# Performance work log

Hardware: AMD Instinct MI355X
Metric: run time of the kernel (lower is better)

Reference implementation:

```python
import jax, jax.numpy as jnp
import numpy as np

B, C, D, H, W = 2, 128, 16, 16, 16

def setup_inputs() -> dict:
    key = jax.random.key(0)
    ks = jax.random.split(key, 7)
    s = 0.02
    return {
        "x": jax.random.normal(ks[0], (B, C, D, H, W), jnp.float32),
        "Wq": jax.random.normal(ks[1], (C, C), jnp.float32) * s,
        "bq": jax.random.normal(ks[2], (C,), jnp.float32) * s,
        "Wk": jax.random.normal(ks[3], (C, C), jnp.float32) * s,
        "bk": jax.random.normal(ks[4], (C,), jnp.float32) * s,
        "Wv": jax.random.normal(ks[5], (C, C), jnp.float32) * s,
        "bv": jax.random.normal(ks[6], (C,), jnp.float32) * s,
    }

def reference(x, Wq, bq, Wk, bk, Wv, bv):
    b, c, d, h, w = x.shape
    n = d * h * w
    xf = x.reshape(b, c, n)  # [B, C, N]
    # 1x1x1 Conv3d == per-voxel linear over channels
    q = jnp.einsum('oc,bcn->bon', Wq, xf) + bq[None, :, None]
    k = jnp.einsum('oc,bcn->bon', Wk, xf) + bk[None, :, None]
    v = jnp.einsum('oc,bcn->bon', Wv, xf) + bv[None, :, None]
    # energy[b,n,m] = sum_c q[b,c,n] * k[b,c,m]  (no scale, as in source)
    energy = jnp.einsum('bcn,bcm->bnm', q, k)
    attention = jax.nn.softmax(energy, axis=-1)
    # out[b,c,n] = sum_m v[b,c,m] * attention[b,n,m]
    out = jnp.einsum('bcm,bnm->bcn', v, attention)
    return out.reshape(b, c, d, h, w)
```

## Files before the change

kernel.cpp:

```cpp
#include <hip/hip_runtime.h>


typedef __bf16 bf16x8 __attribute__((ext_vector_type(8)));
typedef __bf16 bf16x4v __attribute__((ext_vector_type(4)));
typedef float  f32x4  __attribute__((ext_vector_type(4)));

#define LDP 136
#define LDV 72
#define LDO 33

constexpr int CB = 128;
constexpr int NB = 4096;
constexpr int BB = 2;

__device__ __forceinline__ bf16x8 ldfrag(const __bf16* lds, int row, int koff, int ld) {
  return *(const bf16x8*)(lds + row * ld + koff);
}

__device__ __forceinline__ unsigned cvt_pk_bf16(float lo, float hi) {
  unsigned w;
  asm("v_cvt_pk_bf16_f32 %0, %1, %2" : "=v"(w) : "v"(lo), "v"(hi));
  return w;
}

__global__ __launch_bounds__(256) void qkv_proj_kernel(
    const float* __restrict__ x,
    const float* __restrict__ Wq, const float* __restrict__ bq,
    const float* __restrict__ Wk, const float* __restrict__ bk,
    const float* __restrict__ Wv, const float* __restrict__ bv,
    __bf16* __restrict__ Qt, __bf16* __restrict__ Kt, __bf16* __restrict__ Vo)
{
  extern __shared__ __align__(16) char smem_raw[];
  __bf16* xT = (__bf16*)smem_raw;
  __bf16* Wl = xT + 64 * LDP;

  const int b  = blockIdx.y;
  const int n0 = blockIdx.x * 64;
  const int m  = blockIdx.z;
  const int t  = threadIdx.x;
  const int lane = t & 63, w = t >> 6;
  const int l15 = lane & 15, quad = lane >> 4;

  const float* W = (m == 0) ? Wq : (m == 1) ? Wk : Wv;
  const float* bias_p = (m == 0) ? bq : (m == 1) ? bk : bv;
  const float qscale = (m == 0) ? 1.4426950408889634f : 1.0f;

  for (int v = t; v < 2048; v += 256) {
    int c = v >> 4, i4 = v & 15;
    float4 d = *(const float4*)(x + (b * CB + c) * NB + n0 + i4 * 4);
    xT[(i4 * 4 + 0) * LDP + c] = (__bf16)d.x;
    xT[(i4 * 4 + 1) * LDP + c] = (__bf16)d.y;
    xT[(i4 * 4 + 2) * LDP + c] = (__bf16)d.z;
    xT[(i4 * 4 + 3) * LDP + c] = (__bf16)d.w;
  }
  for (int v = t; v < 4096; v += 256) {
    int o = v >> 5, c4 = v & 31;
    float4 d = *(const float4*)(W + o * 128 + c4 * 4);
    bf16x4v u = {(__bf16)d.x, (__bf16)d.y, (__bf16)d.z, (__bf16)d.w};
    *(bf16x4v*)(Wl + o * LDP + c4 * 4) = u;
  }
  __syncthreads();

  if (m < 2) {
    f32x4 acc[8];
#pragma unroll
    for (int ct = 0; ct < 8; ct++) acc[ct] = (f32x4)0.0f;
#pragma unroll
    for (int ks = 0; ks < 4; ks++) {
      int koff = ks * 32 + quad * 8;
      bf16x8 a = ldfrag(xT, w * 16 + l15, koff, LDP);
#pragma unroll
      for (int ct = 0; ct < 8; ct++) {
        bf16x8 bb = ldfrag(Wl, ct * 16 + l15, koff, LDP);
        acc[ct] = __builtin_amdgcn_mfma_f32_16x16x32_bf16(a, bb, acc[ct], 0, 0, 0);
      }
    }
    __bf16* O = (m == 0) ? Qt : Kt;
#pragma unroll
    for (int ct = 0; ct < 8; ct++) {
      int o = ct * 16 + l15;
      float bias = bias_p[o];
#pragma unroll
      for (int r = 0; r < 4; r++) {
        int i = w * 16 + quad * 4 + r;
        O[(b * NB + n0 + i) * CB + o] = (__bf16)((acc[ct][r] + bias) * qscale);
      }
    }
  } else {
    f32x4 acc[2][4];
#pragma unroll
    for (int rr = 0; rr < 2; rr++)
#pragma unroll
      for (int ct = 0; ct < 4; ct++) acc[rr][ct] = (f32x4)0.0f;
#pragma unroll
    for (int ks = 0; ks < 4; ks++) {
      int koff = ks * 32 + quad * 8;
      bf16x8 a0 = ldfrag(Wl, (w * 2 + 0) * 16 + l15, koff, LDP);
      bf16x8 a1 = ldfrag(Wl, (w * 2 + 1) * 16 + l15, koff, LDP);
#pragma unroll
      for (int ct = 0; ct < 4; ct++) {
        bf16x8 bb = ldfrag(xT, ct * 16 + l15, koff, LDP);
        acc[0][ct] = __builtin_amdgcn_mfma_f32_16x16x32_bf16(a0, bb, acc[0][ct], 0, 0, 0);
        acc[1][ct] = __builtin_amdgcn_mfma_f32_16x16x32_bf16(a1, bb, acc[1][ct], 0, 0, 0);
      }
    }
#pragma unroll
    for (int rr = 0; rr < 2; rr++)
#pragma unroll
      for (int ct = 0; ct < 4; ct++)
#pragma unroll
        for (int r = 0; r < 4; r++) {
          int o = (w * 2 + rr) * 16 + quad * 4 + r;
          int i = ct * 16 + l15;
          Vo[(b * CB + o) * NB + n0 + i] = (__bf16)(acc[rr][ct][r] + bias_p[o]);
        }
  }
}

__global__ __launch_bounds__(256, 2) void attn_part_kernel(
    const __bf16* __restrict__ Qt,
    const __bf16* __restrict__ Kt,
    const __bf16* __restrict__ Vo,
    __bf16* __restrict__ Opart, float* __restrict__ Ll, int ksz)
{
  extern __shared__ __align__(16) char smem_raw[];
  __bf16* Kl = (__bf16*)smem_raw;
  __bf16* Vl = Kl + 64 * LDP;
  __bf16* Pl = Vl + 128 * LDV;

  const int b  = blockIdx.y;
  const int q0 = blockIdx.x * 128;
  const int s  = blockIdx.z;
  const int k_base = s * ksz;
  const int nit = ksz >> 6;
  const int t  = threadIdx.x;
  const int lane = t & 63, w = t >> 6;
  const int l15 = lane & 15, quad = lane >> 4;
  const int row0 = w * 32;

  bf16x8 qf[2][4];
#pragma unroll
  for (int qt = 0; qt < 2; qt++)
#pragma unroll
    for (int cb = 0; cb < 4; cb++)
      qf[qt][cb] = *(const bf16x8*)(Qt +
          (size_t)(b * NB + q0 + row0 + qt * 16 + l15) * CB + cb * 32 + quad * 8);

#pragma unroll
  for (int u = 0; u < 4; u++) {
    int v = t + u * 256;
    int j = v >> 4, c8 = v & 15;
    *(bf16x8*)(Kl + j * LDP + c8 * 8) =
        *(const bf16x8*)(Kt + (size_t)(b * NB + k_base + j) * CB + c8 * 8);
  }
#pragma unroll
  for (int u = 0; u < 4; u++) {
    int v = t + u * 256;
    int c = v >> 3, j8 = v & 7;
    *(bf16x8*)(Vl + c * LDV + j8 * 8) =
        *(const bf16x8*)(Vo + (size_t)(b * CB + c) * NB + k_base + j8 * 8);
  }

  float lsum[2] = {0.0f, 0.0f};
  f32x4 o_acc[2][8];
#pragma unroll
  for (int qt = 0; qt < 2; qt++)
#pragma unroll
    for (int tt = 0; tt < 8; tt++) o_acc[qt][tt] = (f32x4)0.0f;

  __syncthreads();

  for (int it = 0; it < nit; it++) {
    bf16x8 kr[4], vr[4];
    if (it + 1 < nit) {
      int m1 = k_base + (it + 1) * 64;
#pragma unroll
      for (int u = 0; u < 4; u++) {
        int v = t + u * 256;
        int j = v >> 4, c8 = v & 15;
        kr[u] = *(const bf16x8*)(Kt + (size_t)(b * NB + m1 + j) * CB + c8 * 8);
      }
#pragma unroll
      for (int u = 0; u < 4; u++) {
        int v = t + u * 256;
        int c = v >> 3, j8 = v & 7;
        vr[u] = *(const bf16x8*)(Vo + (size_t)(b * CB + c) * NB + m1 + j8 * 8);
      }
    }

    f32x4 sacc[2][4];
#pragma unroll
    for (int qt = 0; qt < 2; qt++)
#pragma unroll
      for (int kt = 0; kt < 4; kt++) sacc[qt][kt] = (f32x4)0.0f;

    __builtin_amdgcn_s_setprio(1);
#pragma unroll
    for (int cb = 0; cb < 4; cb++) {
      int koff = cb * 32 + quad * 8;
#pragma unroll
      for (int kt = 0; kt < 4; kt++) {
        bf16x8 af = ldfrag(Kl, kt * 16 + l15, koff, LDP);
        sacc[0][kt] = __builtin_amdgcn_mfma_f32_16x16x32_bf16(af, qf[0][cb], sacc[0][kt], 0, 0, 0);
        sacc[1][kt] = __builtin_amdgcn_mfma_f32_16x16x32_bf16(af, qf[1][cb], sacc[1][kt], 0, 0, 0);
      }
    }
    __builtin_amdgcn_s_setprio(0);

#pragma unroll
    for (int qt = 0; qt < 2; qt++)
#pragma unroll
      for (int kt = 0; kt < 4; kt++) {
        float p0 = exp2f(sacc[qt][kt][0]);
        float p1 = exp2f(sacc[qt][kt][1]);
        float p2 = exp2f(sacc[qt][kt][2]);
        float p3 = exp2f(sacc[qt][kt][3]);
        lsum[qt] += (p0 + p1) + (p2 + p3);
        uint2 u;
        u.x = cvt_pk_bf16(p0, p1);
        u.y = cvt_pk_bf16(p2, p3);
        *(uint2*)(Pl + (row0 + qt * 16 + l15) * LDV + kt * 16 + quad * 4) = u;
      }
    asm volatile("s_waitcnt lgkmcnt(0)" ::: "memory");
    __builtin_amdgcn_sched_barrier(0);

    __builtin_amdgcn_s_setprio(1);
#pragma unroll
    for (int ks = 0; ks < 2; ks++) {
      int koff = ks * 32 + quad * 8;
      bf16x8 a0 = ldfrag(Pl, row0 + l15, koff, LDV);
      bf16x8 a1 = ldfrag(Pl, row0 + 16 + l15, koff, LDV);
#pragma unroll
      for (int tt = 0; tt < 8; tt++) {
        bf16x8 bb = ldfrag(Vl, tt * 16 + l15, koff, LDV);
        o_acc[0][tt] = __builtin_amdgcn_mfma_f32_16x16x32_bf16(a0, bb, o_acc[0][tt], 0, 0, 0);
        o_acc[1][tt] = __builtin_amdgcn_mfma_f32_16x16x32_bf16(a1, bb, o_acc[1][tt], 0, 0, 0);
      }
    }
    __builtin_amdgcn_s_setprio(0);

    if (it + 1 < nit) {
      __syncthreads();
#pragma unroll
      for (int u = 0; u < 4; u++) {
        int v = t + u * 256;
        int j = v >> 4, c8 = v & 15;
        *(bf16x8*)(Kl + j * LDP + c8 * 8) = kr[u];
      }
#pragma unroll
      for (int u = 0; u < 4; u++) {
        int v = t + u * 256;
        int c = v >> 3, j8 = v & 7;
        *(bf16x8*)(Vl + c * LDV + j8 * 8) = vr[u];
      }
      __syncthreads();
    }
  }

#pragma unroll
  for (int qt = 0; qt < 2; qt++) {
    lsum[qt] += __shfl_xor(lsum[qt], 16);
    lsum[qt] += __shfl_xor(lsum[qt], 32);
  }

  const size_t obase = ((size_t)(s * BB + b) * NB + q0) * CB;
#pragma unroll
  for (int qt = 0; qt < 2; qt++)
#pragma unroll
    for (int tt = 0; tt < 8; tt++)
#pragma unroll
      for (int r = 0; r < 4; r++)
        Opart[obase + (size_t)(row0 + qt * 16 + quad * 4 + r) * CB + tt * 16 + l15] =
            (__bf16)o_acc[qt][tt][r];
  if (quad == 0) {
    const size_t lbase = (size_t)(s * BB + b) * NB + q0 + row0;
#pragma unroll
    for (int qt = 0; qt < 2; qt++)
      Ll[lbase + qt * 16 + l15] = lsum[qt];
  }
}

__global__ __launch_bounds__(256) void combine_kernel(
    const __bf16* __restrict__ Opart, const float* __restrict__ Ll,
    float* __restrict__ out, int nsplit)
{
  extern __shared__ __align__(16) char smem_raw[];
  float* Olf = (float*)smem_raw;

  const int b  = blockIdx.y;
  const int n0 = blockIdx.x * 64;
  const int c0 = blockIdx.z * 32;
  const int t  = threadIdx.x;
  const int i  = t >> 2;
  const int cc = (t & 3) * 8;

  float L = 0.0f;
  for (int s = 0; s < nsplit; s++)
    L += Ll[(size_t)(s * BB + b) * NB + n0 + i];

  float acc[8];
#pragma unroll
  for (int u = 0; u < 8; u++) acc[u] = 0.0f;
  for (int s = 0; s < nsplit; s++) {
    bf16x8 d = *(const bf16x8*)(Opart +
        ((size_t)(s * BB + b) * NB + n0 + i) * CB + c0 + cc);
#pragma unroll
    for (int u = 0; u < 8; u++) acc[u] += (float)d[u];
  }
  float invL = 1.0f / L;
#pragma unroll
  for (int u = 0; u < 8; u++) Olf[i * LDO + cc + u] = acc[u] * invL;
  __syncthreads();

  for (int v = t; v < 512; v += 256) {
    int c = v >> 4, i4 = v & 15;
    float4 d;
    d.x = Olf[(i4 * 4 + 0) * LDO + c];
    d.y = Olf[(i4 * 4 + 1) * LDO + c];
    d.z = Olf[(i4 * 4 + 2) * LDO + c];
    d.w = Olf[(i4 * 4 + 3) * LDO + c];
    *(float4*)(out + (size_t)(b * CB + c0 + c) * NB + n0 + i4 * 4) = d;
  }
}

extern "C" void kernel_launch(void* const* d_in, const int* in_sizes, int n_in,
                              void* d_out, int out_size, void* d_ws, size_t ws_size,
                              hipStream_t stream) {
  const float* x  = (const float*)d_in[0];
  const float* Wq = (const float*)d_in[1];
  const float* bq = (const float*)d_in[2];
  const float* Wk = (const float*)d_in[3];
  const float* bk = (const float*)d_in[4];
  const float* Wv = (const float*)d_in[5];
  const float* bv = (const float*)d_in[6];
  float* out = (float*)d_out;

  const size_t qkv_elems = (size_t)BB * NB * CB;
  __bf16* Qt = (__bf16*)d_ws;
  __bf16* Kt = Qt + qkv_elems;
  __bf16* Vo = Kt + qkv_elems;
  char* ws_tail = (char*)(Vo + qkv_elems);
  size_t tail_sz = ws_size - 3 * qkv_elems * sizeof(__bf16);

  const size_t per_split = (size_t)BB * NB * CB * 2 + (size_t)BB * NB * 4;
  int nsplit = 8;
  while (nsplit > 1 && (size_t)nsplit * per_split > tail_sz) nsplit >>= 1;

  __bf16* Opart = (__bf16*)ws_tail;
  float*  Ll = (float*)(Opart + (size_t)nsplit * BB * NB * CB);
  const int ksz = NB / nsplit;

  const int qkv_smem  = (64 * LDP + 128 * LDP) * 2;
  const int attn_smem = (64 * LDP + 128 * LDV + 128 * LDV) * 2;
  const int comb_smem = 64 * LDO * 4;

  qkv_proj_kernel<<<dim3(NB / 64, BB, 3), 256, qkv_smem, stream>>>(
      x, Wq, bq, Wk, bk, Wv, bv, Qt, Kt, Vo);
  attn_part_kernel<<<dim3(NB / 128, BB, nsplit), 256, attn_smem, stream>>>(
      Qt, Kt, Vo, Opart, Ll, ksz);
  combine_kernel<<<dim3(NB / 64, BB, 4), 256, comb_smem, stream>>>(
      Opart, Ll, out, nsplit);
}
```

Measured before the change: 113.7 us.

## Double-buffer K/V tiles with XOR swizzle and keep P in registers via permlane

```diff
diff --git a/kernel.cpp b/kernel.cpp
--- a/kernel.cpp
+++ b/kernel.cpp
@@ -6,7 +6,6 @@
 typedef float  f32x4  __attribute__((ext_vector_type(4)));
 
 #define LDP 136
-#define LDV 72
 #define LDO 33
 
 constexpr int CB = 128;
@@ -124,9 +123,6 @@
     __bf16* __restrict__ Opart, float* __restrict__ Ll, int ksz)
 {
   extern __shared__ __align__(16) char smem_raw[];
-  __bf16* Kl = (__bf16*)smem_raw;
-  __bf16* Vl = Kl + 64 * LDP;
-  __bf16* Pl = Vl + 128 * LDV;
 
   const int b  = blockIdx.y;
   const int q0 = blockIdx.x * 128;
@@ -137,6 +133,7 @@
   const int lane = t & 63, w = t >> 6;
   const int l15 = lane & 15, quad = lane >> 4;
   const int row0 = w * 32;
+  const int xsw = (l15 & 7) << 4;
 
   bf16x8 qf[2][4];
 #pragma unroll
@@ -146,20 +143,37 @@
       qf[qt][cb] = *(const bf16x8*)(Qt +
           (size_t)(b * NB + q0 + row0 + qt * 16 + l15) * CB + cb * 32 + quad * 8);
 
-#pragma unroll
-  for (int u = 0; u < 4; u++) {
-    int v = t + u * 256;
-    int j = v >> 4, c8 = v & 15;
-    *(bf16x8*)(Kl + j * LDP + c8 * 8) =
-        *(const bf16x8*)(Kt + (size_t)(b * NB + k_base + j) * CB + c8 * 8);
-  }
-#pragma unroll
-  for (int u = 0; u < 4; u++) {
-    int v = t + u * 256;
-    int c = v >> 3, j8 = v & 7;
-    *(bf16x8*)(Vl + c * LDV + j8 * 8) =
-        *(const bf16x8*)(Vo + (size_t)(b * CB + c) * NB + k_base + j8 * 8);
-  }
+  bf16x8 kr[4], vr[4];
+  auto load_tile = [&](int m0) {
+#pragma unroll
+    for (int u = 0; u < 4; u++) {
+      int v = t + u * 256;
+      int j = v >> 4, c8 = v & 15;
+      kr[u] = *(const bf16x8*)(Kt + (size_t)(b * NB + m0 + j) * CB + c8 * 8);
+    }
+#pragma unroll
+    for (int u = 0; u < 4; u++) {
+      int v = t + u * 256;
+      int c = v >> 3, j8 = v & 7;
+      vr[u] = *(const bf16x8*)(Vo + (size_t)(b * CB + c) * NB + m0 + j8 * 8);
+    }
+  };
+  auto write_tile = [&](int bf) {
+    char* Kn = smem_raw + bf * 32768;
+    char* Vn = Kn + 16384;
+#pragma unroll
+    for (int u = 0; u < 4; u++) {
+      int v = t + u * 256;
+      int j = v >> 4, c8 = v & 15;
+      *(bf16x8*)(Kn + j * 256 + ((c8 * 16) ^ ((j & 7) << 4))) = kr[u];
+    }
+#pragma unroll
+    for (int u = 0; u < 4; u++) {
+      int v = t + u * 256;
+      int c = v >> 3, j8 = v & 7;
+      *(bf16x8*)(Vn + c * 128 + ((j8 * 16) ^ ((c & 7) << 4))) = vr[u];
+    }
+  };
 
   float lsum[2] = {0.0f, 0.0f};
   f32x4 o_acc[2][8];
@@ -168,47 +182,37 @@
 #pragma unroll
     for (int tt = 0; tt < 8; tt++) o_acc[qt][tt] = (f32x4)0.0f;
 
+  load_tile(k_base);
+  write_tile(0);
   __syncthreads();
 
+  int cur = 0;
   for (int it = 0; it < nit; it++) {
-    bf16x8 kr[4], vr[4];
-    if (it + 1 < nit) {
-      int m1 = k_base + (it + 1) * 64;
-#pragma unroll
-      for (int u = 0; u < 4; u++) {
-        int v = t + u * 256;
-        int j = v >> 4, c8 = v & 15;
-        kr[u] = *(const bf16x8*)(Kt + (size_t)(b * NB + m1 + j) * CB + c8 * 8);
-      }
-#pragma unroll
-      for (int u = 0; u < 4; u++) {
-        int v = t + u * 256;
-        int c = v >> 3, j8 = v & 7;
-        vr[u] = *(const bf16x8*)(Vo + (size_t)(b * CB + c) * NB + m1 + j8 * 8);
-      }
-    }
+    if (it + 1 < nit) load_tile(k_base + (it + 1) * 64);
+
+    const char* Kc = smem_raw + cur * 32768;
+    const char* Vc = Kc + 16384;
 
     f32x4 sacc[2][4];
 #pragma unroll
     for (int qt = 0; qt < 2; qt++)
 #pragma unroll
       for (int kt = 0; kt < 4; kt++) sacc[qt][kt] = (f32x4)0.0f;
-
-    __builtin_amdgcn_s_setprio(1);
 #pragma unroll
     for (int cb = 0; cb < 4; cb++) {
-      int koff = cb * 32 + quad * 8;
+      const int xo = (cb * 64 + quad * 16) ^ xsw;
 #pragma unroll
       for (int kt = 0; kt < 4; kt++) {
-        bf16x8 af = ldfrag(Kl, kt * 16 + l15, koff, LDP);
+        bf16x8 af = *(const bf16x8*)(Kc + (kt * 16 + l15) * 256 + xo);
         sacc[0][kt] = __builtin_amdgcn_mfma_f32_16x16x32_bf16(af, qf[0][cb], sacc[0][kt], 0, 0, 0);
         sacc[1][kt] = __builtin_amdgcn_mfma_f32_16x16x32_bf16(af, qf[1][cb], sacc[1][kt], 0, 0, 0);
       }
     }
-    __builtin_amdgcn_s_setprio(0);
-
-#pragma unroll
-    for (int qt = 0; qt < 2; qt++)
+
+    bf16x8 pa[2][2];
+#pragma unroll
+    for (int qt = 0; qt < 2; qt++) {
+      unsigned d[4][2];
 #pragma unroll
       for (int kt = 0; kt < 4; kt++) {
         float p0 = exp2f(sacc[qt][kt][0]);
@@ -216,44 +220,38 @@
         float p2 = exp2f(sacc[qt][kt][2]);
         float p3 = exp2f(sacc[qt][kt][3]);
         lsum[qt] += (p0 + p1) + (p2 + p3);
-        uint2 u;
-        u.x = cvt_pk_bf16(p0, p1);
-        u.y = cvt_pk_bf16(p2, p3);
-        *(uint2*)(Pl + (row0 + qt * 16 + l15) * LDV + kt * 16 + quad * 4) = u;
-      }
-    asm volatile("s_waitcnt lgkmcnt(0)" ::: "memory");
-    __builtin_amdgcn_sched_barrier(0);
-
-    __builtin_amdgcn_s_setprio(1);
+        d[kt][0] = cvt_pk_bf16(p0, p1);
+        d[kt][1] = cvt_pk_bf16(p2, p3);
+      }
+#pragma unroll
+      for (int ks = 0; ks < 2; ks++) {
+        unsigned a0 = d[2 * ks][0], a1 = d[2 * ks][1];
+        unsigned b0 = d[2 * ks + 1][0], b1 = d[2 * ks + 1][1];
+        asm("v_permlane32_swap_b32 %0, %1" : "+v"(a0), "+v"(b0));
+        asm("v_permlane16_swap_b32 %0, %1" : "+v"(a0), "+v"(b0));
+        asm("v_permlane32_swap_b32 %0, %1" : "+v"(a1), "+v"(b1));
+        asm("v_permlane16_swap_b32 %0, %1" : "+v"(a1), "+v"(b1));
+        union { unsigned u[4]; bf16x8 v; } pk;
+        pk.u[0] = a0; pk.u[1] = a1; pk.u[2] = b0; pk.u[3] = b1;
+        pa[qt][ks] = pk.v;
+      }
+    }
+
 #pragma unroll
     for (int ks = 0; ks < 2; ks++) {
-      int koff = ks * 32 + quad * 8;
-      bf16x8 a0 = ldfrag(Pl, row0 + l15, koff, LDV);
-      bf16x8 a1 = ldfrag(Pl, row0 + 16 + l15, koff, LDV);
+      const int xo = (ks * 64 + quad * 16) ^ xsw;
 #pragma unroll
       for (int tt = 0; tt < 8; tt++) {
-        bf16x8 bb = ldfrag(Vl, tt * 16 + l15, koff, LDV);
-        o_acc[0][tt] = __builtin_amdgcn_mfma_f32_16x16x32_bf16(a0, bb, o_acc[0][tt], 0, 0, 0);
-        o_acc[1][tt] = __builtin_amdgcn_mfma_f32_16x16x32_bf16(a1, bb, o_acc[1][tt], 0, 0, 0);
-      }
-    }
-    __builtin_amdgcn_s_setprio(0);
+        bf16x8 bb = *(const bf16x8*)(Vc + (tt * 16 + l15) * 128 + xo);
+        o_acc[0][tt] = __builtin_amdgcn_mfma_f32_16x16x32_bf16(pa[0][ks], bb, o_acc[0][tt], 0, 0, 0);
+        o_acc[1][tt] = __builtin_amdgcn_mfma_f32_16x16x32_bf16(pa[1][ks], bb, o_acc[1][tt], 0, 0, 0);
+      }
+    }
 
     if (it + 1 < nit) {
+      write_tile(cur ^ 1);
       __syncthreads();
-#pragma unroll
-      for (int u = 0; u < 4; u++) {
-        int v = t + u * 256;
-        int j = v >> 4, c8 = v & 15;
-        *(bf16x8*)(Kl + j * LDP + c8 * 8) = kr[u];
-      }
-#pragma unroll
-      for (int u = 0; u < 4; u++) {
-        int v = t + u * 256;
-        int c = v >> 3, j8 = v & 7;
-        *(bf16x8*)(Vl + c * LDV + j8 * 8) = vr[u];
-      }
-      __syncthreads();
+      cur ^= 1;
     }
   }
 
@@ -351,7 +349,7 @@
   const int ksz = NB / nsplit;
 
   const int qkv_smem  = (64 * LDP + 128 * LDP) * 2;
-  const int attn_smem = (64 * LDP + 128 * LDV + 128 * LDV) * 2;
+  const int attn_smem = 65536;
   const int comb_smem = 64 * LDO * 4;
 
   qkv_proj_kernel<<<dim3(NB / 64, BB, 3), 256, qkv_smem, stream>>>(
```

Measured after the change: 112.4 us. No clear change (-1.1%).
